# Kernel optimization log

Measured on AMD Instinct MI355X. Metric: run time of the kernel, lower is better.

## Reference

```python
import jax, jax.numpy as jnp
import numpy as np

B, T, C, H, N = 4, 2048, 1024, 16, 64
CHUNK = 256           # chunk_len
NBSWA = 2             # n_bswa_chunks
BSWA = CHUNK * NBSWA  # sliding window length
SSTATE = CHUNK        # kvm state slots (chunk_len * n_max_d_chunks)
SINK = 1              # sink_len
PARTIAL = 32          # rope_partial_dim
NEG = -1e30


def _ln(x, w, b, eps=1e-5):
    m = x.mean(-1, keepdims=True)
    v = jnp.mean((x - m) ** 2, -1, keepdims=True)
    return (x - m) * jax.lax.rsqrt(v + eps) * w + b


def _rope_tables():
    freq = (1.0 / 10000.0) ** np.linspace(0.0, 1.0, PARTIAL // 2, dtype=np.float32)
    freq = np.repeat(freq, 2)
    freq = np.concatenate([freq, np.zeros(N - PARTIAL, np.float32)])
    th = np.arange(T, dtype=np.float32)[:, None] * freq[None, :]
    cos = np.cos(th)
    sin = np.sin(th)
    sin[:, 1::2] *= -1.0
    return jnp.asarray(cos), jnp.asarray(sin)


def _rope(x, cos, sin):
    # pairwise flip (x0,x1)->(x1,x0)
    xf = x.reshape(*x.shape[:-1], N // 2, 2)[..., ::-1].reshape(x.shape)
    return cos[None, :, None, :] * x + sin[None, :, None, :] * xf


def _forward(residual, x, v1, x0, dx0,
             Wq, Wk, Wv, Wproj, Wkw,
             x_q, x_k, x_v, lamb,
             ln_q_w, ln_q_b, ln_k_w, ln_k_b, ln_dk_w, ln_dk_b, ln_res_w, ln_res_b,
             front_temp, state_temp):
    q = x @ Wq.T
    k = x @ Wk.T
    v = x @ Wv.T
    v = (1.0 - lamb) * v + lamb * v1  # value residual
    q = q.reshape(B, T, H, N)
    k = k.reshape(B, T, H, N)
    v = v.reshape(B, T, H, N)
    q = _ln(q, ln_q_w, ln_q_b)
    k = _ln(k, ln_k_w, ln_k_b)

    def shift(t):  # token shift (use_dkys=True variant)
        return jnp.concatenate([t[:, 0:1], t[:, :-1]], axis=1)

    q = q + x_q[None, None] * (shift(q) - q)
    k = k + x_k[None, None] * (shift(k) - k)
    v = v + x_v[None, None] * (shift(v) - v)

    cos, sin = _rope_tables()
    q = _rope(q, cos, sin)
    k = _rope(k, cos, sin)

    q = q.transpose(0, 2, 1, 3)  # [B,H,T,N]
    k = k.transpose(0, 2, 1, 3)
    v = v.transpose(0, 2, 1, 3)

    kw = jax.nn.sigmoid(jnp.einsum('btc,hc->bht', x, Wkw))[..., None]  # [B,H,T,1]
    st = state_temp.reshape(1, H, 1, 1)
    ft = front_temp.reshape(1, H, 1, 1)

    d_k = jnp.zeros((B, H, SSTATE, N), x.dtype)
    d_v = jnp.zeros((B, H, SSTATE, N), x.dtype)
    d_cnt = jnp.zeros((B, H, SSTATE, 1), x.dtype)
    scale = 1.0 / np.sqrt(N)
    outs = []
    for e in range(CHUNK, T + 1, CHUNK):  # fixed 8 chunks
        qb = e - CHUNK
        bb = max(0, e - BSWA)
        qc = q[:, :, qb:e]
        c_k = k[:, :, bb:bb + CHUNK]
        c_v = v[:, :, bb:bb + CHUNK]
        bk = k[:, :, bb:e]
        bv = v[:, :, bb:e]

        d_k_norm = _ln(d_k, ln_dk_w, ln_dk_b)
        d_vlen = d_cnt  # running count of accumulated c_v vectors per slot
        v_state = d_v / jnp.clip(jnp.linalg.norm(d_v, axis=-1, keepdims=True), 1e-12) * d_vlen
        k_star = jnp.concatenate([d_k_norm * st, bk * ft], axis=-2)
        v_star = jnp.concatenate([v_state, bv], axis=-2)

        qi = np.arange(qb, e)
        ki = np.arange(bb, e)
        mbias = np.where(ki[None, :] <= qi[:, None], 0.0, NEG).astype(np.float32)
        bias = jnp.asarray(np.concatenate([np.zeros((CHUNK, SSTATE), np.float32), mbias], axis=1))

        sc = jnp.einsum('bhqd,bhkd->bhqk', qc, k_star) * scale + bias
        out = jnp.einsum('bhqk,bhkd->bhqd', jax.nn.softmax(sc, axis=-1), v_star)
        outs.append(out)

        # state update: rope_zeroing on first PARTIAL channels, ln_d_k, nearest-slot scatter
        ck0 = jnp.concatenate([jnp.zeros_like(c_k[..., :PARTIAL]), c_k[..., PARTIAL:]], axis=-1)
        ck0 = _ln(ck0, ln_dk_w, ln_dk_b)
        sim = jnp.einsum('bhcd,bhsd->bhcs', ck0, d_k_norm)
        sim = sim.at[..., 0:SINK].set(NEG)
        kwc = kw[:, :, bb:bb + CHUNK]
        ck0 = ck0 * kwc
        cvw = c_v * kwc
        best = jnp.argmax(sim, axis=-1)                       # [B,H,CHUNK]
        oh = jax.nn.one_hot(best, SSTATE, dtype=x.dtype)      # [B,H,CHUNK,S]
        d_k = d_k + jnp.einsum('bhcs,bhcd->bhsd', oh, ck0)
        d_v = d_v + jnp.einsum('bhcs,bhcd->bhsd', oh, cvw)
        d_cnt = d_cnt + oh.sum(axis=2)[..., None]

    y = jnp.concatenate(outs, axis=2).transpose(0, 2, 1, 3).reshape(B, T, C)
    y = _ln(y, ln_res_w, ln_res_b)
    return residual + y @ Wproj.T


def setup_inputs() -> dict:
    key = jax.random.key(0)
    ks = jax.random.split(key, 12)
    f = lambda k, s, sc=1.0: jax.random.normal(k, s, dtype=jnp.float32) * sc
    return {
        'residual': f(ks[0], (B, T, C)),
        'x': f(ks[1], (B, T, C)),
        'v1': f(ks[2], (B, T, C)),
        'x0': f(ks[3], (B, T, C)),
        'dx0': f(ks[4], (B, T, C)),
        'token_ids': jax.random.randint(ks[5], (B, T), 0, 50257),
        'Wq': f(ks[6], (C, C), 0.02),
        'Wk': f(ks[7], (C, C), 0.02),
        'Wv': f(ks[8], (C, C), 0.02),
        'Wproj': f(ks[9], (C, C), 0.02),
        'Wkw': f(ks[10], (H, C), 0.02),
        'x_q': 0.5 * jnp.ones((H, N), jnp.float32),
        'x_k': 0.5 * jnp.ones((H, N), jnp.float32),
        'x_v': 0.5 * jnp.ones((H, N), jnp.float32),
        'lamb': jnp.float32(0.5),
        'ln_q_w': jnp.ones((N,), jnp.float32), 'ln_q_b': jnp.zeros((N,), jnp.float32),
        'ln_k_w': jnp.ones((N,), jnp.float32), 'ln_k_b': jnp.zeros((N,), jnp.float32),
        'ln_dk_w': jnp.ones((N,), jnp.float32), 'ln_dk_b': jnp.zeros((N,), jnp.float32),
        'ln_res_w': jnp.ones((C,), jnp.float32), 'ln_res_b': jnp.zeros((C,), jnp.float32),
        'front_temp': jnp.ones((H,), jnp.float32),
        'state_temp': jnp.ones((H,), jnp.float32),
    }


def reference(residual, x, v1, x0, dx0, token_ids,
              Wq, Wk, Wv, Wproj, Wkw, x_q, x_k, x_v, lamb,
              ln_q_w, ln_q_b, ln_k_w, ln_k_b, ln_dk_w, ln_dk_b, ln_res_w, ln_res_b,
              front_temp, state_temp):
    del token_ids  # unused in visible forward body
    return _forward(residual, x, v1, x0, dx0,
                    Wq, Wk, Wv, Wproj, Wkw,
                    x_q, x_k, x_v, lamb,
                    ln_q_w, ln_q_b, ln_k_w, ln_k_b, ln_dk_w, ln_dk_b, ln_res_w, ln_res_b,
                    front_temp, state_temp)
```

## Files before the change

kernel.cpp:

```cpp
#include <hip/hip_runtime.h>
#include <math.h>

#define Bq 4
#define Tq 2048
#define Cq 1024
#define Hq 16
#define Nq 64

typedef __attribute__((ext_vector_type(8))) short short8v;
typedef __attribute__((ext_vector_type(4))) float f32x4;

__device__ inline float waveSum(float v) {
#pragma unroll
  for (int o = 32; o; o >>= 1) v += __shfl_xor(v, o);
  return v;
}
__device__ inline unsigned short f2bf(float f) {
  unsigned u = __float_as_uint(f);
  unsigned r = (u + 0x7FFFu + ((u >> 16) & 1u)) >> 16;
  return (unsigned short)r;
}
__device__ inline float bf2f(unsigned short b) {
  return __uint_as_float(((unsigned)b) << 16);
}

__global__ __launch_bounds__(256) void f32_to_bf16_kernel(
    const float* __restrict__ src, unsigned short* __restrict__ dst, int n4)
{
  int i = blockIdx.x * 256 + threadIdx.x;
  if (i >= n4) return;
  float4 v = ((const float4*)src)[i];
  ushort4 o;
  o.x = f2bf(v.x); o.y = f2bf(v.y); o.z = f2bf(v.z); o.w = f2bf(v.w);
  ((ushort4*)dst)[i] = o;
}

__global__ __launch_bounds__(256) void f32_to_bf16_hilo_kernel(
    const float* __restrict__ src, unsigned short* __restrict__ hi,
    unsigned short* __restrict__ lo, int n4)
{
  int i = blockIdx.x * 256 + threadIdx.x;
  if (i >= n4) return;
  float4 v = ((const float4*)src)[i];
  ushort4 h, l;
  h.x = f2bf(v.x); l.x = f2bf(v.x - bf2f(h.x));
  h.y = f2bf(v.y); l.y = f2bf(v.y - bf2f(h.y));
  h.z = f2bf(v.z); l.z = f2bf(v.z - bf2f(h.z));
  h.w = f2bf(v.w); l.w = f2bf(v.w - bf2f(h.w));
  ((ushort4*)hi)[i] = h;
  ((ushort4*)lo)[i] = l;
}

__global__ __launch_bounds__(256) void gemm_bf16(
    const unsigned short* __restrict__ A, const unsigned short* __restrict__ W,
    float* __restrict__ dst, const float* __restrict__ extra,
    const float* __restrict__ lamb_p, int mode)
{
  const int m0 = blockIdx.x * 128, n0 = blockIdx.y * 128;
  const int tid = threadIdx.x;
  const int w = tid >> 6, l = tid & 63;
  const int wr = w >> 1, wc = w & 1;
  const int lrow = l & 15;
  const int lk = (l >> 4) * 8;

  f32x4 acc[4][4];
#pragma unroll
  for (int i = 0; i < 4; ++i)
#pragma unroll
    for (int j = 0; j < 4; ++j) acc[i][j] = (f32x4){0.f, 0.f, 0.f, 0.f};

  const unsigned short* Ab = A + (((size_t)(m0 + wr * 64 + lrow)) << 10) + lk;
  const unsigned short* Wb = W + (((size_t)(n0 + wc * 64 + lrow)) << 10) + lk;

  for (int k0 = 0; k0 < 1024; k0 += 32) {
    short8v a[4], b[4];
#pragma unroll
    for (int i = 0; i < 4; ++i) a[i] = *(const short8v*)(Ab + (((size_t)i) << 14) + k0);
#pragma unroll
    for (int j = 0; j < 4; ++j) b[j] = *(const short8v*)(Wb + (((size_t)j) << 14) + k0);
#pragma unroll
    for (int i = 0; i < 4; ++i)
#pragma unroll
      for (int j = 0; j < 4; ++j)
        acc[i][j] = __builtin_amdgcn_mfma_f32_16x16x32_bf16(a[i], b[j], acc[i][j], 0, 0, 0);
  }

  const float lam = (mode == 2) ? lamb_p[0] : 0.0f;
#pragma unroll
  for (int i = 0; i < 4; ++i)
#pragma unroll
    for (int j = 0; j < 4; ++j)
#pragma unroll
      for (int rg = 0; rg < 4; ++rg) {
        int m = m0 + wr * 64 + i * 16 + (l >> 4) * 4 + rg;
        int n = n0 + wc * 64 + j * 16 + (l & 15);
        float v = acc[i][j][rg];
        if (mode == 3) {
          dst[(size_t)m * Cq + n] = v + extra[(size_t)m * Cq + n];
        } else {
          if (mode == 2) v = (1.0f - lam) * v + lam * extra[(size_t)m * Cq + n];
          int b = m >> 11, t = m & (Tq - 1);
          int h = n >> 6, nn = n & 63;
          dst[((((size_t)b * Hq + h) * Tq + t) << 6) | nn] = v;
        }
      }
}

__global__ __launch_bounds__(256) void gemm_bf16_split(
    const unsigned short* __restrict__ Ah, const unsigned short* __restrict__ Al,
    const unsigned short* __restrict__ Wh, const unsigned short* __restrict__ Wl,
    float* __restrict__ dst)
{
  const int m0 = blockIdx.x * 128, n0 = blockIdx.y * 128;
  const int tid = threadIdx.x;
  const int w = tid >> 6, l = tid & 63;
  const int wr = w >> 1, wc = w & 1;
  const int lrow = l & 15;
  const int lk = (l >> 4) * 8;

  f32x4 acc[4][4];
#pragma unroll
  for (int i = 0; i < 4; ++i)
#pragma unroll
    for (int j = 0; j < 4; ++j) acc[i][j] = (f32x4){0.f, 0.f, 0.f, 0.f};

  const size_t aoff = (((size_t)(m0 + wr * 64 + lrow)) << 10) + lk;
  const size_t woff = (((size_t)(n0 + wc * 64 + lrow)) << 10) + lk;
  const unsigned short* Ahb = Ah + aoff;
  const unsigned short* Alb = Al + aoff;
  const unsigned short* Whb = Wh + woff;
  const unsigned short* Wlb = Wl + woff;

  for (int k0 = 0; k0 < 1024; k0 += 32) {
    short8v ah[4], al[4], bh[4], bl[4];
#pragma unroll
    for (int i = 0; i < 4; ++i) {
      ah[i] = *(const short8v*)(Ahb + (((size_t)i) << 14) + k0);
      al[i] = *(const short8v*)(Alb + (((size_t)i) << 14) + k0);
    }
#pragma unroll
    for (int j = 0; j < 4; ++j) {
      bh[j] = *(const short8v*)(Whb + (((size_t)j) << 14) + k0);
      bl[j] = *(const short8v*)(Wlb + (((size_t)j) << 14) + k0);
    }
#pragma unroll
    for (int i = 0; i < 4; ++i)
#pragma unroll
      for (int j = 0; j < 4; ++j) {
        acc[i][j] = __builtin_amdgcn_mfma_f32_16x16x32_bf16(ah[i], bh[j], acc[i][j], 0, 0, 0);
        acc[i][j] = __builtin_amdgcn_mfma_f32_16x16x32_bf16(ah[i], bl[j], acc[i][j], 0, 0, 0);
        acc[i][j] = __builtin_amdgcn_mfma_f32_16x16x32_bf16(al[i], bh[j], acc[i][j], 0, 0, 0);
      }
  }

#pragma unroll
  for (int i = 0; i < 4; ++i)
#pragma unroll
    for (int j = 0; j < 4; ++j)
#pragma unroll
      for (int rg = 0; rg < 4; ++rg) {
        int m = m0 + wr * 64 + i * 16 + (l >> 4) * 4 + rg;
        int n = n0 + wc * 64 + j * 16 + (l & 15);
        int b = m >> 11, t = m & (Tq - 1);
        int h = n >> 6, nn = n & 63;
        dst[((((size_t)b * Hq + h) * Tq + t) << 6) | nn] = acc[i][j][rg];
      }
}

__global__ __launch_bounds__(256) void postproc(
    const float* __restrict__ src, float* __restrict__ dst,
    unsigned short* __restrict__ dst_bf,
    const float* __restrict__ lnw, const float* __restrict__ lnb,
    const float* __restrict__ xs_p, int doLNRope)
{
  const int w = threadIdx.x >> 6, lane = threadIdx.x & 63;
  const int row = blockIdx.x * 4 + w;
  const int t = row & (Tq - 1);
  const int h = (row >> 11) & (Hq - 1);
  const size_t base = (size_t)row << 6;
  const size_t pbase = (t > 0) ? base - 64 : base;
  float cur = src[base + lane];
  float prv = src[pbase + lane];
  if (doLNRope) {
    const float lw = lnw[lane], lb = lnb[lane];
    {
      float m = waveSum(cur) * (1.0f / 64.0f);
      float d = cur - m;
      float var = waveSum(d * d) * (1.0f / 64.0f);
      cur = d * rsqrtf(var + 1e-5f) * lw + lb;
    }
    {
      float m = waveSum(prv) * (1.0f / 64.0f);
      float d = prv - m;
      float var = waveSum(d * d) * (1.0f / 64.0f);
      prv = d * rsqrtf(var + 1e-5f) * lw + lb;
    }
  }
  const float xv = xs_p[h * 64 + lane];
  float val = cur + xv * (prv - cur);
  if (doLNRope) {
    float partner = __shfl_xor(val, 1);
    if (lane < 32) {
      int i = lane >> 1;
      float freq = (float)exp((double)i * (-log(10000.0) / 15.0));
      float th = (float)t * freq;
      float c = cosf(th), s = sinf(th);
      val = c * val + ((lane & 1) ? -s : s) * partner;
    }
  }
  if (dst) dst[base + lane] = val;
  if (dst_bf) dst_bf[base + lane] = f2bf(val);
}

__global__ __launch_bounds__(256) void kw_kernel(
    const float* __restrict__ x, const float* __restrict__ Wkw, float* __restrict__ out)
{
  const int bt = blockIdx.x;
  const int tid = threadIdx.x, w = tid >> 6, lane = tid & 63;
  __shared__ float xs[Cq];
  for (int i = tid; i < Cq; i += 256) xs[i] = x[(size_t)bt * Cq + i];
  __syncthreads();
  const int b = bt >> 11, t = bt & (Tq - 1);
  for (int h = w; h < Hq; h += 4) {
    float acc = 0.0f;
    for (int i = lane; i < Cq; i += 64) acc += xs[i] * Wkw[h * Cq + i];
    acc = waveSum(acc);
    if (lane == 0) out[((size_t)(b * Hq + h)) * Tq + t] = 1.0f / (1.0f + expf(-acc));
  }
}

__global__ __launch_bounds__(1024, 4) void state_evolve_kernel(
    const float* __restrict__ kf, const unsigned short* __restrict__ v_bf,
    const float* __restrict__ kwp,
    unsigned short* __restrict__ dkn_bf, unsigned short* __restrict__ vst_bf,
    float* __restrict__ cnt_snap,
    const float* __restrict__ lnw, const float* __restrict__ lnb)
{
  const int bh = blockIdx.x;
  const int tid = threadIdx.x;
  const int s = tid >> 2, qd = tid & 3;
  const int db = qd * 16;
  const size_t seq = (size_t)Tq * Nq;
  const float* kb_ = kf + (size_t)bh * seq;
  const unsigned short* vb_ = v_bf + (size_t)bh * seq;
  const float* kwb = kwp + (size_t)bh * Tq;

  __shared__ float dknT[32 * 260];
  __shared__ float ck0T[32 * 260];
  __shared__ unsigned short VRow[256 * 72];
  __shared__ float Ps[256], Qs[256], aS[256], kwS[256];
  __shared__ float lwS[64], lbS[64];
  __shared__ int best[256];

  if (tid < 64) { lwS[tid] = lnw[tid]; lbS[tid] = lnb[tid]; }

  float dkReg[16], dvReg[16];
#pragma unroll
  for (int i = 0; i < 16; ++i) { dkReg[i] = 0.f; dvReg[i] = 0.f; }
  float cnt = 0.f;
  __syncthreads();

  for (int c = 0; c < 8; ++c) {
    const int e = c * 256 + 256;
    const int bb = (e - 512 > 0) ? (e - 512) : 0;

    {
      float sum = 0.f;
#pragma unroll
      for (int i = 0; i < 16; ++i) sum += dkReg[i];
      sum += __shfl_xor(sum, 1); sum += __shfl_xor(sum, 2);
      const float mean = sum * (1.0f / 64.0f);
      float sq = 0.f;
#pragma unroll
      for (int i = 0; i < 16; ++i) { float d = dkReg[i] - mean; sq += d * d; }
      sq += __shfl_xor(sq, 1); sq += __shfl_xor(sq, 2);
      const float rs = rsqrtf(sq * (1.0f / 64.0f) + 1e-5f);
      float kn[16];
#pragma unroll
      for (int i = 0; i < 16; ++i)
        kn[i] = (dkReg[i] - mean) * rs * lwS[db + i] + lbS[db + i];
      unsigned int pk[8];
#pragma unroll
      for (int i2 = 0; i2 < 8; ++i2)
        pk[i2] = (unsigned)f2bf(kn[2 * i2]) | ((unsigned)f2bf(kn[2 * i2 + 1]) << 16);
      unsigned short* kd = dkn_bf + (((size_t)bh * 8 + c) << 14) + s * 64 + db;
      *(uint4*)kd = make_uint4(pk[0], pk[1], pk[2], pk[3]);
      *(uint4*)(kd + 8) = make_uint4(pk[4], pk[5], pk[6], pk[7]);

      if (c < 7) {
        if (qd >= 2) {
#pragma unroll
          for (int i = 0; i < 16; ++i) dknT[(db - 32 + i) * 260 + s] = kn[i];
        } else {
          float pp = 0.f, qq = 0.f;
#pragma unroll
          for (int i = 0; i < 16; ++i) {
            pp += kn[i] * lwS[db + i];
            qq += kn[i] * lbS[db + i];
          }
          pp += __shfl_xor(pp, 1);
          qq += __shfl_xor(qq, 1);
          if (qd == 0) { Ps[s] = pp; Qs[s] = qq; }
        }
      }

      float sqv = 0.f;
#pragma unroll
      for (int i = 0; i < 16; ++i) sqv += dvReg[i] * dvReg[i];
      sqv += __shfl_xor(sqv, 1); sqv += __shfl_xor(sqv, 2);
      const float inrm = 1.0f / fmaxf(sqrtf(sqv), 1e-12f);
#pragma unroll
      for (int i2 = 0; i2 < 8; ++i2)
        pk[i2] = (unsigned)f2bf(dvReg[2 * i2] * inrm) |
                 ((unsigned)f2bf(dvReg[2 * i2 + 1] * inrm) << 16);
      unsigned short* vd = vst_bf + (((size_t)bh * 8 + c) << 14) + s * 64 + db;
      *(uint4*)vd = make_uint4(pk[0], pk[1], pk[2], pk[3]);
      *(uint4*)(vd + 8) = make_uint4(pk[4], pk[5], pk[6], pk[7]);
      if (qd == 0) cnt_snap[((size_t)bh * 8 + c) * 256 + s] = cnt;
    }

    if (c == 7) break;

    {
      float kv[16];
      if (qd >= 2) {
        const float* krow = kb_ + (size_t)(bb + s) * 64 + db;
#pragma unroll
        for (int i = 0; i < 16; i += 4) {
          float4 t4 = *(const float4*)(krow + i);
          kv[i] = t4.x; kv[i + 1] = t4.y; kv[i + 2] = t4.z; kv[i + 3] = t4.w;
        }
      } else {
#pragma unroll
        for (int i = 0; i < 16; ++i) kv[i] = 0.f;
      }
      float sum = 0.f;
#pragma unroll
      for (int i = 0; i < 16; ++i) sum += kv[i];
      sum += __shfl_xor(sum, 1); sum += __shfl_xor(sum, 2);
      const float mean = sum * (1.0f / 64.0f);
      float sq = 0.f;
#pragma unroll
      for (int i = 0; i < 16; ++i) { float d = kv[i] - mean; sq += d * d; }
      sq += __shfl_xor(sq, 1); sq += __shfl_xor(sq, 2);
      const float rs = rsqrtf(sq * (1.0f / 64.0f) + 1e-5f);
      if (qd >= 2) {
#pragma unroll
        for (int i = 0; i < 16; ++i)
          ck0T[(db - 32 + i) * 260 + s] =
              (kv[i] - mean) * rs * lwS[db + i] + lbS[db + i];
      }
      if (qd == 0) {
        aS[s] = (0.0f - mean) * rs;
        kwS[s] = kwb[bb + s];
      }
      const unsigned short* vsrc = vb_ + (size_t)(bb + s) * 64 + db;
      *(uint4*)&VRow[s * 72 + db] = *(const uint4*)vsrc;
      *(uint4*)&VRow[s * 72 + db + 8] = *(const uint4*)(vsrc + 8);
    }
    __syncthreads();

    {
      const int tx = tid & 31, ty = tid >> 5;
#pragma unroll
      for (int pass = 0; pass < 2; ++pass) {
        const int rc0 = pass * 128 + ty * 4;
        float a4[4];
#pragma unroll
        for (int i = 0; i < 4; ++i) a4[i] = aS[rc0 + i];
        float acc[4][8];
#pragma unroll
        for (int j = 0; j < 8; ++j) {
          const float pj = Ps[tx + 32 * j], qj = Qs[tx + 32 * j];
#pragma unroll
          for (int i = 0; i < 4; ++i) acc[i][j] = a4[i] * pj + qj;
        }
#pragma unroll 8
        for (int k = 0; k < 32; ++k) {
          f32x4 av = *(const f32x4*)&ck0T[k * 260 + rc0];
          float bv[8];
#pragma unroll
          for (int j = 0; j < 8; ++j) bv[j] = dknT[k * 260 + tx + 32 * j];
#pragma unroll
          for (int i = 0; i < 4; ++i)
#pragma unroll
            for (int j = 0; j < 8; ++j) acc[i][j] += av[i] * bv[j];
        }
#pragma unroll
        for (int i = 0; i < 4; ++i) {
          float bvv = -3.0e38f;
          int bi = 1 << 30;
#pragma unroll
          for (int j = 0; j < 8; ++j) {
            int s2 = tx + 32 * j;
            float v = acc[i][j];
            if (s2 == 0) v = -1.0e30f;
            if (v > bvv || (v == bvv && s2 < bi)) { bvv = v; bi = s2; }
          }
#pragma unroll
          for (int o = 16; o; o >>= 1) {
            float ov = __shfl_xor(bvv, o);
            int oi = __shfl_xor(bi, o);
            if (ov > bvv || (ov == bvv && oi < bi)) { bvv = ov; bi = oi; }
          }
          if (tx == 0) best[rc0 + i] = bi;
        }
      }
    }
    __syncthreads();

    {
      int cadd = 0;
      for (int rc = 0; rc < 256; ++rc) {
        if (best[rc] == s) {
          const float kwv = kwS[rc];
          if (qd < 2) {
            const float a = aS[rc];
#pragma unroll
            for (int i = 0; i < 16; ++i)
              dkReg[i] += (a * lwS[db + i] + lbS[db + i]) * kwv;
          } else {
#pragma unroll
            for (int i = 0; i < 16; ++i)
              dkReg[i] += ck0T[(db - 32 + i) * 260 + rc] * kwv;
          }
          const uint4 u0 = *(const uint4*)&VRow[rc * 72 + db];
          const uint4 u1 = *(const uint4*)&VRow[rc * 72 + db + 8];
          const unsigned uu[8] = {u0.x, u0.y, u0.z, u0.w, u1.x, u1.y, u1.z, u1.w};
#pragma unroll
          for (int i2 = 0; i2 < 8; ++i2) {
            dvReg[2 * i2] += __uint_as_float((uu[i2] & 0xFFFFu) << 16) * kwv;
            dvReg[2 * i2 + 1] += __uint_as_float(uu[i2] & 0xFFFF0000u) * kwv;
          }
          ++cadd;
        }
      }
      cnt += (float)cadd;
    }
    __syncthreads();
  }
}

__global__ __launch_bounds__(256, 2) void attn_mfma_kernel(
    const unsigned short* __restrict__ q_bf, const unsigned short* __restrict__ k_bf,
    const unsigned short* __restrict__ v_bf,
    const unsigned short* __restrict__ dkn_bf, const unsigned short* __restrict__ vst_bf,
    const float* __restrict__ cnt_snap, float* __restrict__ y,
    const float* __restrict__ ftp, const float* __restrict__ stp)
{
  const int blk = blockIdx.x;
  const int bh = blk >> 4;
  const int c = (blk >> 1) & 7;
  const int half = blk & 1;
  const int h = bh & (Hq - 1);
  const int tid = threadIdx.x;
  const int w = tid >> 6, l = tid & 63;
  const int g = l >> 4, n = l & 15;
  const int rows0 = c * 256 + half * 128 + w * 32;
  const int e = c * 256 + 256;
  const int bb = (e - 512 > 0) ? (e - 512) : 0;
  const int nwt = (e - bb) >> 6;
  const float stsc = stp[h] * 0.125f, ftsc = ftp[h] * 0.125f;
  const size_t seq = (size_t)Tq * Nq;

  __shared__ unsigned short Ks[64 * 72];
  __shared__ unsigned short VTs[64 * 72];
  __shared__ unsigned short Ps[4][32 * 72];
  __shared__ float wts[64];

  short8v qf[2][2];
#pragma unroll
  for (int mt = 0; mt < 2; ++mt)
#pragma unroll
    for (int kh = 0; kh < 2; ++kh)
      qf[mt][kh] = *(const short8v*)(q_bf + (size_t)bh * seq +
                                     (size_t)(rows0 + mt * 16 + n) * 64 + kh * 32 + g * 8);

  f32x4 oacc[2][4];
#pragma unroll
  for (int mt = 0; mt < 2; ++mt)
#pragma unroll
    for (int dt = 0; dt < 4; ++dt) oacc[mt][dt] = (f32x4){0.f, 0.f, 0.f, 0.f};
  float rowM[2][4], rowL[2][4];
#pragma unroll
  for (int mt = 0; mt < 2; ++mt)
#pragma unroll
    for (int r = 0; r < 4; ++r) { rowM[mt][r] = -1.0e30f; rowL[mt][r] = 0.f; }

  const int nkt = 4 + nwt;
  for (int kt = 0; kt < nkt; ++kt) {
    const bool isState = kt < 4;
    const int t0 = isState ? kt * 64 : bb + (kt - 4) * 64;
    const unsigned short* ksrc = isState
        ? dkn_bf + (((size_t)bh * 8 + c) << 14) + (size_t)t0 * 64
        : k_bf + (size_t)bh * seq + (size_t)t0 * 64;
    const unsigned short* vsrc = isState
        ? vst_bf + (((size_t)bh * 8 + c) << 14) + (size_t)t0 * 64
        : v_bf + (size_t)bh * seq + (size_t)t0 * 64;

    __syncthreads();
    {
      const int row = tid >> 2, q4 = tid & 3;
      const unsigned short* src = ksrc + row * 64 + q4 * 16;
      *(uint4*)&Ks[row * 72 + q4 * 16] = *(const uint4*)src;
      *(uint4*)&Ks[row * 72 + q4 * 16 + 8] = *(const uint4*)(src + 8);
      const unsigned short* vs = vsrc + row * 64 + q4 * 16;
#pragma unroll
      for (int i = 0; i < 16; ++i) VTs[(q4 * 16 + i) * 72 + row] = vs[i];
      if (tid < 64)
        wts[tid] = isState ? cnt_snap[((size_t)bh * 8 + c) * 256 + kt * 64 + tid] : 1.0f;
    }
    __syncthreads();

    f32x4 sacc[2][4];
#pragma unroll
    for (int mt = 0; mt < 2; ++mt)
#pragma unroll
      for (int nt = 0; nt < 4; ++nt) sacc[mt][nt] = (f32x4){0.f, 0.f, 0.f, 0.f};
#pragma unroll
    for (int nt = 0; nt < 4; ++nt) {
      short8v kf0 = *(const short8v*)&Ks[(nt * 16 + n) * 72 + g * 8];
      short8v kf1 = *(const short8v*)&Ks[(nt * 16 + n) * 72 + 32 + g * 8];
#pragma unroll
      for (int mt = 0; mt < 2; ++mt) {
        sacc[mt][nt] = __builtin_amdgcn_mfma_f32_16x16x32_bf16(qf[mt][0], kf0, sacc[mt][nt], 0, 0, 0);
        sacc[mt][nt] = __builtin_amdgcn_mfma_f32_16x16x32_bf16(qf[mt][1], kf1, sacc[mt][nt], 0, 0, 0);
      }
    }

    const float scale = isState ? stsc : ftsc;
    float wt_n[4];
#pragma unroll
    for (int nt = 0; nt < 4; ++nt) wt_n[nt] = wts[nt * 16 + n];

#pragma unroll
    for (int mt = 0; mt < 2; ++mt) {
#pragma unroll
      for (int r = 0; r < 4; ++r) {
        float sv[4];
#pragma unroll
        for (int nt = 0; nt < 4; ++nt) {
          float s = sacc[mt][nt][r] * scale;
          if (!isState) {
            int qi = rows0 + mt * 16 + g * 4 + r;
            int kj = t0 + nt * 16 + n;
            if (kj > qi) s = -1.0e30f;
          }
          sv[nt] = s;
        }
        float tmax = fmaxf(fmaxf(sv[0], sv[1]), fmaxf(sv[2], sv[3]));
        tmax = fmaxf(tmax, __shfl_xor(tmax, 1));
        tmax = fmaxf(tmax, __shfl_xor(tmax, 2));
        tmax = fmaxf(tmax, __shfl_xor(tmax, 4));
        tmax = fmaxf(tmax, __shfl_xor(tmax, 8));
        const float Mold = rowM[mt][r];
        const float Mnew = fmaxf(Mold, tmax);
        const float al = __expf(Mold - Mnew);
        rowM[mt][r] = Mnew;
        float p[4], ts = 0.f;
#pragma unroll
        for (int nt = 0; nt < 4; ++nt) { p[nt] = __expf(sv[nt] - Mnew); ts += p[nt]; }
        ts += __shfl_xor(ts, 1);
        ts += __shfl_xor(ts, 2);
        ts += __shfl_xor(ts, 4);
        ts += __shfl_xor(ts, 8);
        rowL[mt][r] = rowL[mt][r] * al + ts;
#pragma unroll
        for (int dt = 0; dt < 4; ++dt) oacc[mt][dt][r] *= al;
        const int prow = (mt * 16 + g * 4 + r) * 72;
#pragma unroll
        for (int nt = 0; nt < 4; ++nt)
          Ps[w][prow + nt * 16 + n] = f2bf(p[nt] * wt_n[nt]);
      }
    }

    short8v pf[2][2];
#pragma unroll
    for (int mt = 0; mt < 2; ++mt)
#pragma unroll
      for (int jh = 0; jh < 2; ++jh)
        pf[mt][jh] = *(const short8v*)&Ps[w][(mt * 16 + n) * 72 + jh * 32 + g * 8];
#pragma unroll
    for (int dt = 0; dt < 4; ++dt) {
      short8v vf0 = *(const short8v*)&VTs[(dt * 16 + n) * 72 + g * 8];
      short8v vf1 = *(const short8v*)&VTs[(dt * 16 + n) * 72 + 32 + g * 8];
#pragma unroll
      for (int mt = 0; mt < 2; ++mt) {
        oacc[mt][dt] = __builtin_amdgcn_mfma_f32_16x16x32_bf16(pf[mt][0], vf0, oacc[mt][dt], 0, 0, 0);
        oacc[mt][dt] = __builtin_amdgcn_mfma_f32_16x16x32_bf16(pf[mt][1], vf1, oacc[mt][dt], 0, 0, 0);
      }
    }
  }

#pragma unroll
  for (int mt = 0; mt < 2; ++mt) {
#pragma unroll
    for (int r = 0; r < 4; ++r) {
      const float inv = 1.0f / rowL[mt][r];
      const int row = rows0 + mt * 16 + g * 4 + r;
#pragma unroll
      for (int dt = 0; dt < 4; ++dt)
        y[(size_t)bh * seq + (size_t)row * 64 + dt * 16 + n] = oacc[mt][dt][r] * inv;
    }
  }
}

__global__ __launch_bounds__(256) void final_ln(
    const float* __restrict__ y, const float* __restrict__ lnw,
    const float* __restrict__ lnb, unsigned short* __restrict__ dst)
{
  const int bt = blockIdx.x;
  const int b = bt >> 11, t = bt & (Tq - 1);
  const int tid = threadIdx.x, w = tid >> 6, lane = tid & 63;
  __shared__ float red[8];
  float v[4];
  float s = 0.0f;
#pragma unroll
  for (int i = 0; i < 4; ++i) {
    int c = tid + (i << 8);
    int h = c >> 6, n = c & 63;
    v[i] = y[((((size_t)b * Hq + h) * Tq + t) << 6) + n];
    s += v[i];
  }
  s = waveSum(s);
  if (lane == 0) red[w] = s;
  __syncthreads();
  const float mean = (red[0] + red[1] + red[2] + red[3]) * (1.0f / 1024.0f);
  float s2 = 0.0f;
#pragma unroll
  for (int i = 0; i < 4; ++i) { float d = v[i] - mean; s2 += d * d; }
  s2 = waveSum(s2);
  if (lane == 0) red[4 + w] = s2;
  __syncthreads();
  const float var = (red[4] + red[5] + red[6] + red[7]) * (1.0f / 1024.0f);
  const float rs = rsqrtf(var + 1e-5f);
#pragma unroll
  for (int i = 0; i < 4; ++i) {
    int c = tid + (i << 8);
    dst[(size_t)bt * Cq + c] = f2bf((v[i] - mean) * rs * lnw[c] + lnb[c]);
  }
}

extern "C" void kernel_launch(void* const* d_in, const int* in_sizes, int n_in,
                              void* d_out, int out_size, void* d_ws, size_t ws_size,
                              hipStream_t stream)
{
  (void)in_sizes; (void)n_in; (void)out_size; (void)ws_size;
  const float* residual = (const float*)d_in[0];
  const float* x        = (const float*)d_in[1];
  const float* v1       = (const float*)d_in[2];
  const float* Wq       = (const float*)d_in[6];
  const float* Wk       = (const float*)d_in[7];
  const float* Wv       = (const float*)d_in[8];
  const float* Wproj    = (const float*)d_in[9];
  const float* Wkw      = (const float*)d_in[10];
  const float* x_q      = (const float*)d_in[11];
  const float* x_k      = (const float*)d_in[12];
  const float* x_v      = (const float*)d_in[13];
  const float* lamb     = (const float*)d_in[14];
  const float* ln_q_w   = (const float*)d_in[15];
  const float* ln_q_b   = (const float*)d_in[16];
  const float* ln_k_w   = (const float*)d_in[17];
  const float* ln_k_b   = (const float*)d_in[18];
  const float* ln_dk_w  = (const float*)d_in[19];
  const float* ln_dk_b  = (const float*)d_in[20];
  const float* ln_res_w = (const float*)d_in[21];
  const float* ln_res_b = (const float*)d_in[22];
  const float* ftp      = (const float*)d_in[23];
  const float* stp      = (const float*)d_in[24];

  float* ws = (float*)d_ws;
  const size_t SZ = (size_t)Bq * Hq * Tq * Nq;
  float* q_raw = ws;
  float* ybuf  = ws;
  float* k_raw = ws + SZ;
  unsigned short* vst_bf = (unsigned short*)(ws + SZ);
  float* cnt_snap = ws + SZ + SZ / 2;
  float* v_mix = ws + 2 * SZ;
  unsigned short* ylnb_bf = (unsigned short*)(ws + 2 * SZ);
  float* k_fin = ws + 3 * SZ;
  unsigned short* q_bf = (unsigned short*)(ws + 4 * SZ);
  unsigned short* x_lo = q_bf;
  unsigned short* k_bf = q_bf + SZ;
  unsigned short* wk_hi = k_bf;
  unsigned short* wk_lo = wk_hi + (1u << 20);
  unsigned short* v_bf = (unsigned short*)(ws + 5 * SZ);
  unsigned short* xb   = v_bf + SZ;
  unsigned short* dkn_bf = xb;
  unsigned short* wqb = (unsigned short*)(ws + 6 * SZ);
  unsigned short* wvb = wqb + (1u << 20);
  unsigned short* wpb = wvb + (1u << 20);
  float* kwbuf = ws + 6 * SZ + ((3u << 20) >> 1);

  dim3 gb(256);
  dim3 ggb(64, 8);

  hipLaunchKernelGGL(f32_to_bf16_hilo_kernel, dim3((int)(SZ / 4 / 256)), gb, 0, stream,
                     x, xb, x_lo, (int)(SZ / 4));
  hipLaunchKernelGGL(f32_to_bf16_hilo_kernel, dim3(1024), gb, 0, stream,
                     Wk, wk_hi, wk_lo, 262144);
  hipLaunchKernelGGL(f32_to_bf16_kernel, dim3(1024), gb, 0, stream, Wq, wqb, 262144);
  hipLaunchKernelGGL(f32_to_bf16_kernel, dim3(1024), gb, 0, stream, Wv, wvb, 262144);
  hipLaunchKernelGGL(f32_to_bf16_kernel, dim3(1024), gb, 0, stream, Wproj, wpb, 262144);

  hipLaunchKernelGGL(gemm_bf16, ggb, gb, 0, stream, xb, wqb, q_raw, (const float*)nullptr, lamb, 1);
  hipLaunchKernelGGL(gemm_bf16_split, ggb, gb, 0, stream, xb, x_lo, wk_hi, wk_lo, k_raw);
  hipLaunchKernelGGL(gemm_bf16, ggb, gb, 0, stream, xb, wvb, v_mix, v1, lamb, 2);
  hipLaunchKernelGGL(kw_kernel, dim3(Bq * Tq), gb, 0, stream, x, Wkw, kwbuf);

  const int rows = Bq * Hq * Tq;
  hipLaunchKernelGGL(postproc, dim3(rows / 4), gb, 0, stream, q_raw, (float*)nullptr, q_bf, ln_q_w, ln_q_b, x_q, 1);
  hipLaunchKernelGGL(postproc, dim3(rows / 4), gb, 0, stream, k_raw, k_fin, k_bf, ln_k_w, ln_k_b, x_k, 1);
  hipLaunchKernelGGL(postproc, dim3(rows / 4), gb, 0, stream, v_mix, (float*)nullptr, v_bf,
                     (const float*)nullptr, (const float*)nullptr, x_v, 0);

  hipLaunchKernelGGL(state_evolve_kernel, dim3(Bq * Hq), dim3(1024), 0, stream,
                     k_fin, v_bf, kwbuf, dkn_bf, vst_bf, cnt_snap, ln_dk_w, ln_dk_b);

  hipLaunchKernelGGL(attn_mfma_kernel, dim3(Bq * Hq * 16), gb, 0, stream,
                     q_bf, k_bf, v_bf, dkn_bf, vst_bf, cnt_snap, ybuf, ftp, stp);

  hipLaunchKernelGGL(final_ln, dim3(Bq * Tq), gb, 0, stream, ybuf, ln_res_w, ln_res_b, ylnb_bf);
  hipLaunchKernelGGL(gemm_bf16, ggb, gb, 0, stream, ylnb_bf, wpb, (float*)d_out, residual, lamb, 3);
}
```

Before: 1.378 ms.

## Skip argmax on first chunk of state_evolve, vectorize best-slot scan

For chunk 0 the state is zero, so the argmax similarity is skipped and every row is assigned slot 1 directly, which removes the matmul and reduction work for that chunk. The loop that scans best[] now reads four entries at a time with int4 loads. Launch bounds drop from 4 to 1 blocks per multiprocessor, which gives the compiler more registers. A dead 8-row accumulator loop is also added, which the compiler will likely remove. Assuming slot 1 on the first chunk relies on the tie-breaking when all scores are equal, and the __syncthreads now sits inside a branch that is uniform across the block.

```diff
diff --git a/kernel.cpp b/kernel.cpp
--- a/kernel.cpp
+++ b/kernel.cpp
@@ -229,7 +229,7 @@
   }
 }
 
-__global__ __launch_bounds__(1024, 4) void state_evolve_kernel(
+__global__ __launch_bounds__(1024, 1) void state_evolve_kernel(
     const float* __restrict__ kf, const unsigned short* __restrict__ v_bf,
     const float* __restrict__ kwp,
     unsigned short* __restrict__ dkn_bf, unsigned short* __restrict__ vst_bf,
@@ -287,7 +287,7 @@
       *(uint4*)kd = make_uint4(pk[0], pk[1], pk[2], pk[3]);
       *(uint4*)(kd + 8) = make_uint4(pk[4], pk[5], pk[6], pk[7]);
 
-      if (c < 7) {
+      if (c > 0 && c < 7) {
         if (qd >= 2) {
 #pragma unroll
           for (int i = 0; i < 16; ++i) dknT[(db - 32 + i) * 260 + s] = kn[i];
@@ -357,14 +357,30 @@
       const unsigned short* vsrc = vb_ + (size_t)(bb + s) * 64 + db;
       *(uint4*)&VRow[s * 72 + db] = *(const uint4*)vsrc;
       *(uint4*)&VRow[s * 72 + db + 8] = *(const uint4*)(vsrc + 8);
+      if (c == 0 && tid < 256) best[tid] = 1;
     }
     __syncthreads();
 
-    {
+    if (c > 0) {
       const int tx = tid & 31, ty = tid >> 5;
 #pragma unroll
       for (int pass = 0; pass < 2; ++pass) {
-        const int rc0 = pass * 128 + ty * 4;
+        const int rc0 = pass * 128 + ty * 8;
+        float a4[8];
+#pragma unroll
+        for (int i = 0; i < 8; ++i) a4[i] = aS[rc0 + i];
+        float acc[8][8];
+#pragma unroll
+        for (int j = 0; j < 8; ++j) {
+          const float pj = Ps[tx + 32 * j], qj = Qs[tx + 32 * j];
+#pragma unroll
+          for (int i = 0; i < 8; ++i) acc[i][j] = a4[i] * pj + qj;
+        }
+        (void)acc;
+      }
+#pragma unroll
+      for (int pass = 0; pass < 2; ++pass) {
+        const int rc0 = pass * 128 + (tid >> 5) * 4;
         float a4[4];
 #pragma unroll
         for (int i = 0; i < 4; ++i) a4[i] = aS[rc0 + i];
@@ -406,33 +422,39 @@
           if (tx == 0) best[rc0 + i] = bi;
         }
       }
-    }
-    __syncthreads();
+      __syncthreads();
+    }
 
     {
       int cadd = 0;
-      for (int rc = 0; rc < 256; ++rc) {
-        if (best[rc] == s) {
-          const float kwv = kwS[rc];
-          if (qd < 2) {
-            const float a = aS[rc];
-#pragma unroll
-            for (int i = 0; i < 16; ++i)
-              dkReg[i] += (a * lwS[db + i] + lbS[db + i]) * kwv;
-          } else {
-#pragma unroll
-            for (int i = 0; i < 16; ++i)
-              dkReg[i] += ck0T[(db - 32 + i) * 260 + rc] * kwv;
+      for (int rc4 = 0; rc4 < 64; ++rc4) {
+        const int4 b4 = *(const int4*)&best[rc4 * 4];
+#pragma unroll
+        for (int u = 0; u < 4; ++u) {
+          const int bm = (u == 0) ? b4.x : (u == 1) ? b4.y : (u == 2) ? b4.z : b4.w;
+          if (bm == s) {
+            const int rc = rc4 * 4 + u;
+            const float kwv = kwS[rc];
+            if (qd < 2) {
+              const float a = aS[rc];
+#pragma unroll
+              for (int i = 0; i < 16; ++i)
+                dkReg[i] += (a * lwS[db + i] + lbS[db + i]) * kwv;
+            } else {
+#pragma unroll
+              for (int i = 0; i < 16; ++i)
+                dkReg[i] += ck0T[(db - 32 + i) * 260 + rc] * kwv;
+            }
+            const uint4 u0 = *(const uint4*)&VRow[rc * 72 + db];
+            const uint4 u1 = *(const uint4*)&VRow[rc * 72 + db + 8];
+            const unsigned uu[8] = {u0.x, u0.y, u0.z, u0.w, u1.x, u1.y, u1.z, u1.w};
+#pragma unroll
+            for (int i2 = 0; i2 < 8; ++i2) {
+              dvReg[2 * i2] += __uint_as_float((uu[i2] & 0xFFFFu) << 16) * kwv;
+              dvReg[2 * i2 + 1] += __uint_as_float(uu[i2] & 0xFFFF0000u) * kwv;
+            }
+            ++cadd;
           }
-          const uint4 u0 = *(const uint4*)&VRow[rc * 72 + db];
-          const uint4 u1 = *(const uint4*)&VRow[rc * 72 + db + 8];
-          const unsigned uu[8] = {u0.x, u0.y, u0.z, u0.w, u1.x, u1.y, u1.z, u1.w};
-#pragma unroll
-          for (int i2 = 0; i2 < 8; ++i2) {
-            dvReg[2 * i2] += __uint_as_float((uu[i2] & 0xFFFFu) << 16) * kwv;
-            dvReg[2 * i2 + 1] += __uint_as_float(uu[i2] & 0xFFFF0000u) * kwv;
-          }
-          ++cadd;
         }
       }
       cnt += (float)cadd;
```

Result: no change. 1.381 ms (+0.2%).
